# Performance work log

Measured on AMD Instinct MI355X. Metric: run time of the kernel, lower is better.

The kernel has to match this reference:

```python
import math
import jax, jax.numpy as jnp
import numpy as np

B, S, D, H = 2, 2048, 1024, 16
DH = D // H


def setup_inputs() -> dict:
    key = jax.random.key(0)
    ks = jax.random.split(key, 6)
    scale = 1.0 / math.sqrt(D)  # xavier-ish scale for stability
    inp = {
        "query": jax.random.normal(ks[0], (B, S, D), jnp.float32),
        "mask": jax.random.randint(ks[1], (B, S, S), 0, 2) > 0,
        "Wq": jax.random.normal(ks[2], (D, D), jnp.float32) * scale,
        "bq": jnp.zeros((D,), jnp.float32),
        "Wk": jax.random.normal(ks[3], (D, D), jnp.float32) * scale,
        "bk": jnp.zeros((D,), jnp.float32),
        "Wv": jax.random.normal(ks[4], (D, D), jnp.float32) * scale,
        "bv": jnp.zeros((D,), jnp.float32),
        "Wo": jax.random.normal(ks[5], (D, D), jnp.float32) * scale,
        "bo": jnp.zeros((D,), jnp.float32),
    }
    return inp


def reference(query, mask, Wq, bq, Wk, bk, Wv, bv, Wo, bo):
    # self-attention: memory = query
    def shape(x):  # [B,S,D] -> [B,H,S,DH]
        return x.reshape(B, S, H, DH).transpose(0, 2, 1, 3)

    q = shape(query @ Wq.T + bq) / math.sqrt(DH)
    k = shape(query @ Wk.T + bk)
    v = shape(query @ Wv.T + bv)
    scores = jnp.einsum("bhqd,bhkd->bhqk", q, k)
    scores = jnp.where(mask[:, None, :, :], jnp.float32(-1e18), scores)
    attn = jax.nn.softmax(scores, axis=-1)
    # dropout is identity in eval mode
    ctx = jnp.einsum("bhqk,bhkd->bhqd", attn, v)
    ctx = ctx.transpose(0, 2, 1, 3).reshape(B, S, D)
    return ctx @ Wo.T + bo
```

## Files before the change

### kernel.cpp

```cpp
#include <hip/hip_runtime.h>

#define B_ 2
#define S_ 2048
#define D_ 1024
#define H_ 16
#define DH_ 64

typedef float f32x4 __attribute__((ext_vector_type(4)));
typedef short s16x8 __attribute__((ext_vector_type(8)));
typedef __bf16 bf16x8 __attribute__((ext_vector_type(8)));
typedef unsigned int uint;

template <typename T>
static __device__ auto mfma_sel(T a, T b, f32x4 c, int)
    -> decltype(__builtin_amdgcn_mfma_f32_16x16x32_bf16(a, b, c, 0, 0, 0)) {
  return __builtin_amdgcn_mfma_f32_16x16x32_bf16(a, b, c, 0, 0, 0);
}
template <typename T>
static __device__ f32x4 mfma_sel(T a, T b, f32x4 c, long) {
  return __builtin_amdgcn_mfma_f32_16x16x32_bf16(
      __builtin_bit_cast(bf16x8, a), __builtin_bit_cast(bf16x8, b), c, 0, 0, 0);
}
static __device__ __forceinline__ f32x4 mfma_bf16(s16x8 a, s16x8 b, f32x4 c) {
  return mfma_sel(a, b, c, 0);
}

static __device__ __forceinline__ short f2bf(float f) {
  unsigned u = __float_as_uint(f);
  u += 0x7fffu + ((u >> 16) & 1u);
  return (short)(u >> 16);
}

static __device__ __forceinline__ void async16(const short* g, short* l) {
  __builtin_amdgcn_global_load_lds(
      (const __attribute__((address_space(1))) unsigned int*)g,
      (__attribute__((address_space(3))) unsigned int*)l, 16, 0, 0);
}

__global__ void detect_mask_kernel(const uint* __restrict__ m,
                                   int* __restrict__ flag) {
  int lane = threadIdx.x;
  bool gt1 = false, notf = false;
  for (int i = 0; i < 16; ++i) {
    uint v = m[lane * 16 + i];
    if (v > 1u) gt1 = true;
    if (v != 0u && v != 0x3F800000u) notf = true;
  }
  unsigned long long b1 = __ballot(gt1);
  unsigned long long b2 = __ballot(notf);
  if (lane == 0) {
    int f;
    if (b1 == 0ull) f = 1;
    else if (b2 == 0ull) f = 2;
    else f = 0;
    *flag = f;
  }
}

__global__ __launch_bounds__(256) void build_bitmask_kernel(
    const void* __restrict__ mask, const int* __restrict__ flag,
    uint* __restrict__ bmT) {
  int w = blockIdx.x * 256 + threadIdx.x;
  int b = w >> 17;
  int rem = w & 131071;
  int q = rem >> 6;
  int kt = rem & 63;
  int mty = *flag;
  uint bits = 0;
  if (mty == 0) {
    const uint* p = (const uint*)((const unsigned char*)mask +
                                  ((size_t)b * S_ + q) * S_ + (size_t)kt * 32);
#pragma unroll
    for (int i = 0; i < 8; ++i) {
      uint v = p[i];
#pragma unroll
      for (int j = 0; j < 4; ++j)
        if ((v >> (8 * j)) & 0xffu) bits |= 1u << (i * 4 + j);
    }
  } else {
    const uint* p = (const uint*)mask + ((size_t)b * S_ + q) * S_ + kt * 32;
#pragma unroll
    for (int i = 0; i < 32; ++i)
      if (p[i]) bits |= 1u << i;
  }
  bmT[((size_t)b * (S_ / 32) + kt) * S_ + q] = bits;
}

__global__ __launch_bounds__(256) void convert_kernel(
    const float* __restrict__ q, const float* __restrict__ wq,
    const float* __restrict__ wk, const float* __restrict__ wv,
    short* __restrict__ qbf, short* __restrict__ wqkv) {
  int bid = blockIdx.x;
  int t = threadIdx.x;
  const float* src;
  short* dst;
  int rowbase, seg;
  if (bid < 2048)      { src = q;  dst = qbf;  rowbase = bid * 2;          seg = -1; }
  else if (bid < 2560) { src = wq; dst = wqkv; rowbase = (bid - 2048) * 2; seg = 0; }
  else if (bid < 3072) { src = wk; dst = wqkv; rowbase = (bid - 2560) * 2; seg = 1; }
  else                 { src = wv; dst = wqkv; rowbase = (bid - 3072) * 2; seg = 2; }
  int rl = rowbase + (t >> 7);
  int k = (t & 127) * 8;
  const float* s8 = src + (size_t)rl * 1024 + k;
  f32x4 a = *(const f32x4*)s8;
  f32x4 b = *(const f32x4*)(s8 + 4);
  s16x8 r;
  r[0] = f2bf(a[0]); r[1] = f2bf(a[1]); r[2] = f2bf(a[2]); r[3] = f2bf(a[3]);
  r[4] = f2bf(b[0]); r[5] = f2bf(b[1]); r[6] = f2bf(b[2]); r[7] = f2bf(b[3]);
  int grow = (seg < 0) ? rl : (seg * 1024 + rl);
  size_t chunk = ((size_t)(grow >> 4) * 32 + (k >> 5)) * 64 +
                 ((k >> 3) & 3) * 16 + (grow & 15);
  *(s16x8*)(dst + chunk * 8) = r;
}

__global__ __launch_bounds__(256) void convert_wo_kernel(
    const float* __restrict__ wo, short* __restrict__ wob) {
  size_t i = ((size_t)blockIdx.x * 256 + threadIdx.x) * 8;
  f32x4 a = *(const f32x4*)(wo + i);
  f32x4 b = *(const f32x4*)(wo + i + 4);
  s16x8 r;
  r[0] = f2bf(a[0]); r[1] = f2bf(a[1]); r[2] = f2bf(a[2]); r[3] = f2bf(a[3]);
  r[4] = f2bf(b[0]); r[5] = f2bf(b[1]); r[6] = f2bf(b[2]); r[7] = f2bf(b[3]);
  *(s16x8*)(wob + i) = r;
}

__global__ __launch_bounds__(256) void gemm_qkv_kernel(
    const short* __restrict__ A, const short* __restrict__ Bt,
    const float* __restrict__ bq, const float* __restrict__ bk,
    const float* __restrict__ bv, short* __restrict__ q_ws,
    short* __restrict__ KF, short* __restrict__ VF) {
  __shared__ short lds[8192];
  const int tid = threadIdx.x;
  const int lane = tid & 63;
  const int wave = tid >> 6;
  const int l16 = lane & 15;
  const int quad = lane >> 4;
  const int mb0 = blockIdx.x * 8;
  const int nb0 = blockIdx.y * 8;
  const int m0 = blockIdx.x * 128 + (wave >> 1) * 64;
  const int n0 = blockIdx.y * 128 + (wave & 1) * 64;
  const int g = tid >> 6, c = tid & 63;

  f32x4 acc[4][4];
#pragma unroll
  for (int i = 0; i < 4; ++i)
#pragma unroll
    for (int j = 0; j < 4; ++j) acc[i][j] = (f32x4){0.f, 0.f, 0.f, 0.f};

  for (int kb = 0; kb < 32; ++kb) {
    async16(A + (((size_t)(mb0 + g) * 32 + kb) * 64 + c) * 8, lds + tid * 8);
    async16(A + (((size_t)(mb0 + g + 4) * 32 + kb) * 64 + c) * 8,
            lds + 2048 + tid * 8);
    async16(Bt + (((size_t)(nb0 + g) * 32 + kb) * 64 + c) * 8,
            lds + 4096 + tid * 8);
    async16(Bt + (((size_t)(nb0 + g + 4) * 32 + kb) * 64 + c) * 8,
            lds + 6144 + tid * 8);
    __syncthreads();
    s16x8 a[4], b[4];
#pragma unroll
    for (int i = 0; i < 4; ++i)
      a[i] = *(const s16x8*)(lds + (((wave >> 1) * 4 + i) * 64 + lane) * 8);
#pragma unroll
    for (int j = 0; j < 4; ++j)
      b[j] = *(const s16x8*)(lds + 4096 + (((wave & 1) * 4 + j) * 64 + lane) * 8);
#pragma unroll
    for (int i = 0; i < 4; ++i)
#pragma unroll
      for (int j = 0; j < 4; ++j) acc[i][j] = mfma_bf16(a[i], b[j], acc[i][j]);
    __syncthreads();
  }

#pragma unroll
  for (int i = 0; i < 4; ++i) {
#pragma unroll
    for (int j = 0; j < 4; ++j) {
#pragma unroll
      for (int r = 0; r < 4; ++r) {
        int m = m0 + i * 16 + quad * 4 + r;
        int n = n0 + j * 16 + l16;
        int seg = n >> 10, nl = n & 1023;
        float bias = (seg == 0) ? bq[nl] : ((seg == 1) ? bk[nl] : bv[nl]);
        float v = acc[i][j][r] + bias;
        if (seg == 0) v *= 0.125f;
        int bb = m >> 11, s = m & (S_ - 1);
        int hh = nl >> 6, dh = nl & 63;
        int bh = bb * H_ + hh;
        short bv16 = f2bf(v);
        if (seg == 0) {
          q_ws[((size_t)bh * S_ + s) * DH_ + dh] = bv16;
        } else if (seg == 1) {
          int kt = s >> 5, r5 = s & 31;
          int kkb = r5 >> 4, kl16 = r5 & 15;
          int kf = dh >> 5, qd = (dh >> 3) & 3, e = dh & 7;
          KF[(size_t)bh * 131072 +
             ((size_t)kt * 256 + (kkb * 2 + kf) * 64 + qd * 16 + kl16) * 8 + e] = bv16;
        } else {
          int kt = s >> 5, ko = s & 31;
          int hi = ko >> 4, qd = (ko >> 2) & 3, j4 = ko & 3;
          int nb = dh >> 4, vl16 = dh & 15, e = hi * 4 + j4;
          VF[(size_t)bh * 131072 +
             ((size_t)kt * 256 + nb * 64 + qd * 16 + vl16) * 8 + e] = bv16;
        }
      }
    }
  }
}

__global__ void attn_kernel(
    const short* __restrict__ Q, const short* __restrict__ KF,
    const short* __restrict__ VF, const uint* __restrict__ bmT,
    short* __restrict__ ctx_out) {
  __shared__ short lds[8192];
  const int tid = threadIdx.x;
  const int lane = tid & 63;
  const int wave = tid >> 6;
  const int l16 = lane & 15;
  const int quad = lane >> 4;
  const int bid = blockIdx.x;
  const int bh = bid >> 4;
  const int qt128 = bid & 15;
  const int b = bh >> 4;
  const int h = bh & 15;
  const int qbase = qt128 * 128 + wave * 16;

  const short* Qh = Q + (size_t)bh * S_ * DH_;
  const short* KFb = KF + (size_t)bh * 131072;
  const short* VFb = VF + (size_t)bh * 131072;
  const uint* bmb = bmT + (size_t)b * (S_ / 32) * S_;

  s16x8 qf[2];
#pragma unroll
  for (int kf = 0; kf < 2; ++kf)
    qf[kf] = *(const s16x8*)(Qh + (size_t)(qbase + l16) * DH_ + kf * 32 + quad * 8);

  f32x4 ctx[4];
#pragma unroll
  for (int nb = 0; nb < 4; ++nb) ctx[nb] = (f32x4){0.f, 0.f, 0.f, 0.f};
  float ls = 0.f;

  for (int kt2 = 0; kt2 < S_ / 64; ++kt2) {
    async16(KFb + (size_t)kt2 * 4096 + tid * 8, lds + tid * 8);
    async16(VFb + (size_t)kt2 * 4096 + tid * 8, lds + 4096 + tid * 8);
    uint w[2];
    w[0] = bmb[(size_t)(2 * kt2) * S_ + qbase + l16];
    w[1] = bmb[(size_t)(2 * kt2 + 1) * S_ + qbase + l16];
    __syncthreads();

#pragma unroll
    for (int kbt = 0; kbt < 2; ++kbt) {
      s16x8 ka[2][2];
#pragma unroll
      for (int kb = 0; kb < 2; ++kb)
#pragma unroll
        for (int kf = 0; kf < 2; ++kf)
          ka[kb][kf] =
              *(const s16x8*)(lds + kbt * 2048 + ((kb * 2 + kf) * 64 + lane) * 8);

      f32x4 sc[2];
#pragma unroll
      for (int kb = 0; kb < 2; ++kb) {
        f32x4 t = mfma_bf16(ka[kb][0], qf[0], (f32x4){0.f, 0.f, 0.f, 0.f});
        sc[kb] = mfma_bf16(ka[kb][1], qf[1], t);
      }

      s16x8 pa;
      float sum = 0.f;
#pragma unroll
      for (int kb = 0; kb < 2; ++kb)
#pragma unroll
        for (int r = 0; r < 4; ++r) {
          int bit = (w[kbt] >> (kb * 16 + quad * 4 + r)) & 1;
          float p = bit ? 0.f : __expf(sc[kb][r]);
          sum += p;
          pa[kb * 4 + r] = f2bf(p);
        }
      ls += sum;

#pragma unroll
      for (int nb = 0; nb < 4; ++nb) {
        s16x8 vb =
            *(const s16x8*)(lds + 4096 + kbt * 2048 + (nb * 64 + lane) * 8);
        ctx[nb] = mfma_bf16(pa, vb, ctx[nb]);
      }
    }
    __syncthreads();
  }

  ls += __shfl_xor(ls, 16);
  ls += __shfl_xor(ls, 32);

#pragma unroll
  for (int r = 0; r < 4; ++r) {
    float lr = __shfl(ls, quad * 4 + r);
    float inv = 1.f / lr;
    int srow = qbase + quad * 4 + r;
#pragma unroll
    for (int nb = 0; nb < 4; ++nb) {
      int col = h * DH_ + nb * 16 + l16;
      ctx_out[(size_t)(b * S_ + srow) * D_ + col] = f2bf(ctx[nb][r] * inv);
    }
  }
}

__global__ __launch_bounds__(256) void gemm_final_kernel(
    const short* __restrict__ A, const short* __restrict__ Bt,
    const float* __restrict__ bias, float* __restrict__ out) {
  __shared__ short lds[8192];
  const int tid = threadIdx.x;
  const int lane = tid & 63;
  const int wave = tid >> 6;
  const int l16 = lane & 15;
  const int quad = lane >> 4;
  const int m0 = blockIdx.x * 128;
  const int n0 = blockIdx.y * 128;
  const int g = tid >> 6, c = tid & 63;
  const int r15 = c & 15, qd = c >> 4;

  f32x4 acc[4][4];
#pragma unroll
  for (int i = 0; i < 4; ++i)
#pragma unroll
    for (int j = 0; j < 4; ++j) acc[i][j] = (f32x4){0.f, 0.f, 0.f, 0.f};

  for (int k0 = 0; k0 < 1024; k0 += 32) {
    async16(A + (size_t)(m0 + g * 16 + r15) * 1024 + k0 + qd * 8, lds + tid * 8);
    async16(A + (size_t)(m0 + (g + 4) * 16 + r15) * 1024 + k0 + qd * 8,
            lds + 2048 + tid * 8);
    async16(Bt + (size_t)(n0 + g * 16 + r15) * 1024 + k0 + qd * 8,
            lds + 4096 + tid * 8);
    async16(Bt + (size_t)(n0 + (g + 4) * 16 + r15) * 1024 + k0 + qd * 8,
            lds + 6144 + tid * 8);
    __syncthreads();
    s16x8 a[4], b[4];
#pragma unroll
    for (int i = 0; i < 4; ++i)
      a[i] = *(const s16x8*)(lds + (((wave >> 1) * 4 + i) * 64 + lane) * 8);
#pragma unroll
    for (int j = 0; j < 4; ++j)
      b[j] = *(const s16x8*)(lds + 4096 + (((wave & 1) * 4 + j) * 64 + lane) * 8);
#pragma unroll
    for (int i = 0; i < 4; ++i)
#pragma unroll
      for (int j = 0; j < 4; ++j) acc[i][j] = mfma_bf16(a[i], b[j], acc[i][j]);
    __syncthreads();
  }

  const int mw = m0 + (wave >> 1) * 64;
  const int nw = n0 + (wave & 1) * 64;
#pragma unroll
  for (int i = 0; i < 4; ++i)
#pragma unroll
    for (int j = 0; j < 4; ++j)
#pragma unroll
      for (int r = 0; r < 4; ++r) {
        int m = mw + i * 16 + quad * 4 + r;
        int n = nw + j * 16 + l16;
        out[(size_t)m * 1024 + n] = acc[i][j][r] + bias[n];
      }
}

extern "C" void kernel_launch(void* const* d_in, const int* in_sizes, int n_in,
                              void* d_out, int out_size, void* d_ws,
                              size_t ws_size, hipStream_t stream) {
  const float* query = (const float*)d_in[0];
  const void* mask = d_in[1];
  const float* Wq = (const float*)d_in[2];
  const float* bq = (const float*)d_in[3];
  const float* Wk = (const float*)d_in[4];
  const float* bk = (const float*)d_in[5];
  const float* Wv = (const float*)d_in[6];
  const float* bv = (const float*)d_in[7];
  const float* Wo = (const float*)d_in[8];
  const float* bo = (const float*)d_in[9];

  const size_t NE = (size_t)B_ * S_ * D_;
  short* ws_s = (short*)d_ws;
  short* q_ws = ws_s;
  short* KF = ws_s + NE;
  short* VF = ws_s + 2 * NE;
  short* ctx_ws = ws_s + 3 * NE;
  short* wo_bf = ws_s;
  short* qbf = (short*)d_out;
  short* wqkv = qbf + NE;
  uint* bmT = (uint*)(wqkv + 3145728);
  int* flag = (int*)(bmT + 262144);

  detect_mask_kernel<<<1, 64, 0, stream>>>((const uint*)mask, flag);
  build_bitmask_kernel<<<1024, 256, 0, stream>>>(mask, flag, bmT);
  convert_kernel<<<3584, 256, 0, stream>>>(query, Wq, Wk, Wv, qbf, wqkv);

  gemm_qkv_kernel<<<dim3(32, 24), 256, 0, stream>>>(qbf, wqkv, bq, bk, bv,
                                                    q_ws, KF, VF);

  attn_kernel<<<512, 512, 0, stream>>>(q_ws, KF, VF, bmT, ctx_ws);

  convert_wo_kernel<<<512, 256, 0, stream>>>(Wo, wo_bf);

  gemm_final_kernel<<<dim3(32, 8), 256, 0, stream>>>(ctx_ws, wo_bf, bo,
                                                     (float*)d_out);
}
```

Baseline: 253.5 us.

## Double-buffer K/V tiles in attention and use exp2 with prescaled Q

The attention kernel now double-buffers K/V tiles in LDS, prefetching the next 64-key tile and its mask words while computing the current one. This removes one barrier per iteration and is meant to hide global load latency. Q is now prescaled by log2(e)/8 so the softmax can use the hardware exp2 directly, and bf16 conversion of probabilities uses the native cast. LDS use per block doubles, which could reduce occupancy.

```diff
diff --git a/kernel.cpp b/kernel.cpp
--- a/kernel.cpp
+++ b/kernel.cpp
@@ -29,6 +29,10 @@
   unsigned u = __float_as_uint(f);
   u += 0x7fffu + ((u >> 16) & 1u);
   return (short)(u >> 16);
+}
+
+static __device__ __forceinline__ short f2bf_rn(float f) {
+  return __builtin_bit_cast(short, (__bf16)f);
 }
 
 static __device__ __forceinline__ void async16(const short* g, short* l) {
@@ -181,7 +185,7 @@
         int seg = n >> 10, nl = n & 1023;
         float bias = (seg == 0) ? bq[nl] : ((seg == 1) ? bk[nl] : bv[nl]);
         float v = acc[i][j][r] + bias;
-        if (seg == 0) v *= 0.125f;
+        if (seg == 0) v *= 0.18033688011112042f;
         int bb = m >> 11, s = m & (S_ - 1);
         int hh = nl >> 6, dh = nl & 63;
         int bh = bb * H_ + hh;
@@ -210,7 +214,7 @@
     const short* __restrict__ Q, const short* __restrict__ KF,
     const short* __restrict__ VF, const uint* __restrict__ bmT,
     short* __restrict__ ctx_out) {
-  __shared__ short lds[8192];
+  __shared__ short lds[16384];
   const int tid = threadIdx.x;
   const int lane = tid & 63;
   const int wave = tid >> 6;
@@ -222,6 +226,7 @@
   const int b = bh >> 4;
   const int h = bh & 15;
   const int qbase = qt128 * 128 + wave * 16;
+  const int qcol = qbase + l16;
 
   const short* Qh = Q + (size_t)bh * S_ * DH_;
   const short* KFb = KF + (size_t)bh * 131072;
@@ -231,20 +236,32 @@
   s16x8 qf[2];
 #pragma unroll
   for (int kf = 0; kf < 2; ++kf)
-    qf[kf] = *(const s16x8*)(Qh + (size_t)(qbase + l16) * DH_ + kf * 32 + quad * 8);
+    qf[kf] = *(const s16x8*)(Qh + (size_t)qcol * DH_ + kf * 32 + quad * 8);
 
   f32x4 ctx[4];
 #pragma unroll
   for (int nb = 0; nb < 4; ++nb) ctx[nb] = (f32x4){0.f, 0.f, 0.f, 0.f};
   float ls = 0.f;
 
+  async16(KFb + tid * 8, lds + tid * 8);
+  async16(VFb + tid * 8, lds + 4096 + tid * 8);
+  uint w0 = bmb[qcol];
+  uint w1 = bmb[(size_t)S_ + qcol];
+  __syncthreads();
+
   for (int kt2 = 0; kt2 < S_ / 64; ++kt2) {
-    async16(KFb + (size_t)kt2 * 4096 + tid * 8, lds + tid * 8);
-    async16(VFb + (size_t)kt2 * 4096 + tid * 8, lds + 4096 + tid * 8);
-    uint w[2];
-    w[0] = bmb[(size_t)(2 * kt2) * S_ + qbase + l16];
-    w[1] = bmb[(size_t)(2 * kt2 + 1) * S_ + qbase + l16];
-    __syncthreads();
+    uint wn0 = 0, wn1 = 0;
+    if (kt2 < S_ / 64 - 1) {
+      const int st = ((kt2 & 1) ^ 1) << 13;
+      async16(KFb + (size_t)(kt2 + 1) * 4096 + tid * 8, lds + st + tid * 8);
+      async16(VFb + (size_t)(kt2 + 1) * 4096 + tid * 8,
+              lds + st + 4096 + tid * 8);
+      wn0 = bmb[(size_t)(2 * kt2 + 2) * S_ + qcol];
+      wn1 = bmb[(size_t)(2 * kt2 + 3) * S_ + qcol];
+    }
+    const short* kls = lds + ((kt2 & 1) << 13);
+    const short* vls = kls + 4096;
+    const uint wcur[2] = {w0, w1};
 
 #pragma unroll
     for (int kbt = 0; kbt < 2; ++kbt) {
@@ -254,7 +271,7 @@
 #pragma unroll
         for (int kf = 0; kf < 2; ++kf)
           ka[kb][kf] =
-              *(const s16x8*)(lds + kbt * 2048 + ((kb * 2 + kf) * 64 + lane) * 8);
+              *(const s16x8*)(kls + kbt * 2048 + ((kb * 2 + kf) * 64 + lane) * 8);
 
       f32x4 sc[2];
 #pragma unroll
@@ -269,21 +286,22 @@
       for (int kb = 0; kb < 2; ++kb)
 #pragma unroll
         for (int r = 0; r < 4; ++r) {
-          int bit = (w[kbt] >> (kb * 16 + quad * 4 + r)) & 1;
-          float p = bit ? 0.f : __expf(sc[kb][r]);
+          int bit = (wcur[kbt] >> (kb * 16 + quad * 4 + r)) & 1;
+          float p = bit ? 0.f : __builtin_amdgcn_exp2f(sc[kb][r]);
           sum += p;
-          pa[kb * 4 + r] = f2bf(p);
+          pa[kb * 4 + r] = f2bf_rn(p);
         }
       ls += sum;
 
 #pragma unroll
       for (int nb = 0; nb < 4; ++nb) {
-        s16x8 vb =
-            *(const s16x8*)(lds + 4096 + kbt * 2048 + (nb * 64 + lane) * 8);
+        s16x8 vb = *(const s16x8*)(vls + kbt * 2048 + (nb * 64 + lane) * 8);
         ctx[nb] = mfma_bf16(pa, vb, ctx[nb]);
       }
     }
     __syncthreads();
+    w0 = wn0;
+    w1 = wn1;
   }
 
   ls += __shfl_xor(ls, 16);
```

Result: faster. 241.3 us (-4.8%).
